# Optimization experiments

Hardware: AMD Instinct MI355X
Metric: run time of the kernel (lower is better)

Reference implementation:

```python
import jax, jax.numpy as jnp
import numpy as np

DIM = 1024
NUM_HEADS = 16
HEAD_DIM = DIM // NUM_HEADS
SCALE = DIM ** (-0.5)  # NOTE: original scales by full dim, not head_dim


def setup_inputs() -> dict:
    key = jax.random.key(0)
    ks = jax.random.split(key, 5)
    B, S = 2, 2048
    x = jax.random.normal(ks[0], (B, S, DIM), dtype=jnp.float32)
    w_qkv = jax.random.normal(ks[1], (DIM, 3 * DIM), dtype=jnp.float32) * (DIM ** -0.5)
    b_qkv = jax.random.normal(ks[2], (3 * DIM,), dtype=jnp.float32) * 0.02
    w_proj = jax.random.normal(ks[3], (DIM, DIM), dtype=jnp.float32) * (DIM ** -0.5)
    b_proj = jax.random.normal(ks[4], (DIM,), dtype=jnp.float32) * 0.02
    return {"x": x, "w_qkv": w_qkv, "b_qkv": b_qkv, "w_proj": w_proj, "b_proj": b_proj}


def reference(x, w_qkv, b_qkv, w_proj, b_proj):
    B, S, D = x.shape
    qkv = x @ w_qkv + b_qkv                                  # [B,S,3D]
    qkv = qkv.reshape(B, S, NUM_HEADS, 3 * HEAD_DIM).transpose(0, 2, 1, 3)  # [B,H,S,3hd]
    q, k, v = jnp.split(qkv, 3, axis=-1)                     # each [B,H,S,hd]
    attn = jnp.einsum("bhqd,bhkd->bhqk", q, k) * SCALE       # [B,H,S,S]
    attn = jax.nn.softmax(attn, axis=-1)
    out = jnp.einsum("bhqk,bhkd->bhqd", attn, v)             # [B,H,S,hd]
    out = out.transpose(0, 2, 1, 3).reshape(B, S, D)
    return out @ w_proj + b_proj
```

## Files before the change

### kernel.cpp

```cpp
#include <hip/hip_runtime.h>
#include <hip/hip_bf16.h>

#define DIM 1024
#define NH 16
#define HD 64
#define BB 2
#define SS 2048
#define MROWS (BB * SS)
#define SCALE 0.03125f
#define SC_LOG2E 0.04508422002778011f

typedef unsigned short u16;
typedef unsigned int u32;
typedef __attribute__((ext_vector_type(8))) short short8;
typedef __attribute__((ext_vector_type(4))) float f32x4;
typedef __attribute__((ext_vector_type(2))) unsigned int u32x2;

#if __has_builtin(__builtin_amdgcn_exp2f)
#define EXP2(x) __builtin_amdgcn_exp2f(x)
#else
#define EXP2(x) __builtin_exp2f(x)
#endif

__device__ __forceinline__ u16 f2bf(float f) {
  union { float f; u32 u; } v; v.f = f;
  return (u16)((v.u + 0x7fffu + ((v.u >> 16) & 1u)) >> 16);
}

__device__ __forceinline__ u32 pack2bf(float a, float b) {
  union { __hip_bfloat162 h; u32 u; } cv;
  cv.h = __float22bfloat162_rn(make_float2(a, b));
  return cv.u;
}

__device__ __forceinline__ void plswap32(u32& a, u32& b) {
#if __has_builtin(__builtin_amdgcn_permlane32_swap)
  u32x2 t = __builtin_amdgcn_permlane32_swap(a, b, false, false);
  a = t[0]; b = t[1];
#else
  asm("v_permlane32_swap_b32 %0, %1" : "+v"(a), "+v"(b));
#endif
}
__device__ __forceinline__ void plswap16(u32& a, u32& b) {
#if __has_builtin(__builtin_amdgcn_permlane16_swap)
  u32x2 t = __builtin_amdgcn_permlane16_swap(a, b, false, false);
  a = t[0]; b = t[1];
#else
  asm("v_permlane16_swap_b32 %0, %1" : "+v"(a), "+v"(b));
#endif
}

__device__ __forceinline__ void async16(const u16* g, u16* l) {
  __builtin_amdgcn_global_load_lds(
      (const __attribute__((address_space(1))) void*)(const void*)g,
      (__attribute__((address_space(3))) void*)(void*)l, 16, 0, 0);
}

__device__ __forceinline__ short8 ld8(const u16* p) { return *(const short8*)p; }

__global__ void cvt_kernel(const float* __restrict__ in, u16* __restrict__ out, int n4) {
  int i = blockIdx.x * blockDim.x + threadIdx.x;
  if (i < n4) {
    float4 v = ((const float4*)in)[i];
    u32 lo = (u32)f2bf(v.x) | ((u32)f2bf(v.y) << 16);
    u32 hi = (u32)f2bf(v.z) | ((u32)f2bf(v.w) << 16);
    ((uint2*)out)[i] = make_uint2(lo, hi);
  }
}

__global__ void tconv_kernel(const float* __restrict__ in, u16* __restrict__ out, int R, int C) {
  __shared__ u16 t[64 * 65];
  int c0 = blockIdx.x * 64, r0 = blockIdx.y * 64;
  #pragma unroll
  for (int i = 0; i < 16; i++) {
    int j = i * 256 + threadIdx.x;
    int rr = j >> 6, cc = j & 63;
    t[rr * 65 + cc] = f2bf(in[(size_t)(r0 + rr) * C + c0 + cc]);
  }
  __syncthreads();
  #pragma unroll
  for (int i = 0; i < 16; i++) {
    int j = i * 256 + threadIdx.x;
    int oc = j >> 6, orr = j & 63;
    out[(size_t)(c0 + oc) * R + r0 + orr] = t[orr * 65 + oc];
  }
}

template <int MODE, int BN, int NXB>
__global__ __launch_bounds__(256, (BN == 128 ? 2 : 3)) void gemm_bk64(
    const u16* __restrict__ A, const u16* __restrict__ Bt,
    const float* __restrict__ bias, void* __restrict__ C,
    u16* __restrict__ vT, int M, int N, int K) {
  constexpr int JN = BN / 32;
  constexpr int BTI = BN / 32;
  constexpr int BUF = 8192 + BN * 64;
  __shared__ __align__(16) u16 smem[2 * BUF];
  const int tid = threadIdx.x;
  const int w = tid >> 6, l = tid & 63;
  const int r = l & 15, q = l >> 4;
  const int nwg = gridDim.x;
  const int cpx = nwg >> 3;
  const int lin = blockIdx.x;
  const int swz = (lin & 7) * cpx + (lin >> 3);
  const int m0 = (swz / NXB) * 128, n0 = (swz % NXB) * BN;
  const int qm = (w & 1) * 64, qn = (w >> 1) * (BN / 2);

  const int gc = (l & 7) ^ (l >> 3);
  const size_t aoffb = (size_t)(m0 + w * 32 + (l >> 3)) * K + (size_t)gc * 8;
  const size_t boffb = (size_t)(n0 + w * (BN / 4) + (l >> 3)) * K + (size_t)gc * 8;
  const int xs = r & 7;

#define GSTAGE(K0, BASE) do {                                                    \
    u16* As_ = (BASE); u16* Bs_ = As_ + 8192;                                    \
    _Pragma("unroll")                                                            \
    for (int t = 0; t < 4; t++)                                                  \
      async16(A + aoffb + (size_t)t * 8 * K + (K0), As_ + w * 2048 + t * 512 + l * 8); \
    _Pragma("unroll")                                                            \
    for (int t = 0; t < BTI; t++)                                                \
      async16(Bt + boffb + (size_t)t * 8 * K + (K0), Bs_ + w * (BN * 16) + t * 512 + l * 8); \
  } while (0)

  f32x4 acc[4][JN] = {};
  GSTAGE(0, smem);
  __syncthreads();
  for (int k0 = 0; k0 < K; k0 += 64) {
    u16* As = smem + ((k0 >> 6) & 1) * BUF;
    u16* Bs = As + 8192;
    if (k0 + 64 < K) GSTAGE(k0 + 64, smem + ((((k0 >> 6) & 1) ^ 1) * BUF));
    short8 af[2][4], bfr[2][JN];
    #pragma unroll
    for (int kq = 0; kq < 2; kq++) {
      #pragma unroll
      for (int i = 0; i < 4; i++)
        af[kq][i] = ld8(&As[(qm + i * 16 + r) * 64 + (((kq * 4 + q) ^ xs) * 8)]);
      #pragma unroll
      for (int j = 0; j < JN; j++)
        bfr[kq][j] = ld8(&Bs[(qn + j * 16 + r) * 64 + (((kq * 4 + q) ^ xs) * 8)]);
    }
    #pragma unroll
    for (int kq = 0; kq < 2; kq++)
      #pragma unroll
      for (int i = 0; i < 4; i++)
        #pragma unroll
        for (int j = 0; j < JN; j++)
          acc[i][j] = __builtin_amdgcn_mfma_f32_16x16x32_bf16(af[kq][i], bfr[kq][j], acc[i][j], 0, 0, 0);
    __syncthreads();
  }
#undef GSTAGE
  #pragma unroll
  for (int i = 0; i < 4; i++) {
    int ro = m0 + qm + i * 16 + q * 4;
    #pragma unroll
    for (int j = 0; j < JN; j++) {
      int col = n0 + qn + j * 16 + r;
      float bv = bias[col];
      float v0 = acc[i][j][0] + bv, v1 = acc[i][j][1] + bv;
      float v2 = acc[i][j][2] + bv, v3 = acc[i][j][3] + bv;
      if (MODE == 1) {
        float* out = (float*)C;
        out[(size_t)(ro + 0) * N + col] = v0;
        out[(size_t)(ro + 1) * N + col] = v1;
        out[(size_t)(ro + 2) * N + col] = v2;
        out[(size_t)(ro + 3) * N + col] = v3;
      } else {
        int h = col / 192, wi = col - h * 192;
        if (wi >= 128) {
          int bb = ro >> 11, s = ro & 2047, d = wi - 128;
          uint2 pk = make_uint2(pack2bf(v0, v1), pack2bf(v2, v3));
          *(uint2*)&vT[((size_t)((bb * NH + h) * HD + d)) * SS + s] = pk;
        } else {
          u16* qk2 = (u16*)C;
          const float sc = (wi < 64) ? SC_LOG2E : 1.0f;
          qk2[(size_t)(ro + 0) * 2048 + h * 128 + wi] = f2bf(v0 * sc);
          qk2[(size_t)(ro + 1) * 2048 + h * 128 + wi] = f2bf(v1 * sc);
          qk2[(size_t)(ro + 2) * 2048 + h * 128 + wi] = f2bf(v2 * sc);
          qk2[(size_t)(ro + 3) * 2048 + h * 128 + wi] = f2bf(v3 * sc);
        }
      }
    }
  }
}

__global__ __launch_bounds__(512, 4) void attn6_kernel(
    const u16* __restrict__ qk2, const u16* __restrict__ vT,
    u16* __restrict__ attno) {
  __shared__ __align__(16) u16 smem[32768];
  const int tid = threadIdx.x;
  const int w = tid >> 6, l = tid & 63;
  const int r = l & 15, q = l >> 4;
  const int wq = w & 3, ws = w >> 2;
  const int lin = blockIdx.x + 16 * (blockIdx.y + 16 * blockIdx.z);
  const int k8 = lin & 7, jj = lin >> 3;
  const int bh = ((jj >> 4) << 3) + k8;
  const int h = bh & 15, b = bh >> 4;
  const int q0 = (jj & 15) * 128;

  const u16* qb = qk2 + (size_t)b * SS * 2048;
  const u16* kB = qb + h * 128 + 64;
  const u16* vB = vT + (size_t)((b * NH + h) * HD) * SS;

  short8 qf[2][2];
  #pragma unroll
  for (int i = 0; i < 2; i++)
    #pragma unroll
    for (int kq = 0; kq < 2; kq++)
      qf[i][kq] = ld8(qb + (size_t)(q0 + wq * 32 + i * 16 + r) * 2048 + h * 128 + kq * 32 + q * 8);

  const int klrow = l >> 3;
  const int kchunk = (l & 7) ^ klrow;
  const int vlrow = l >> 4;
  const int vslot = l & 15;

#define STAGE(KV0, DST) do {                                                     \
    u16* Kd_ = (DST); u16* Vd_ = Kd_ + 8192;                                     \
    _Pragma("unroll")                                                            \
    for (int tt = 0; tt < 2; tt++) {                                             \
      int g = w * 2 + tt;                                                        \
      async16(kB + (size_t)((KV0) + g * 8 + klrow) * 2048 + kchunk * 8,          \
              &Kd_[g * 512 + l * 8]);                                            \
    }                                                                            \
    _Pragma("unroll")                                                            \
    for (int tt = 0; tt < 2; tt++) {                                             \
      int g = w * 2 + tt;                                                        \
      int d_ = g * 4 + vlrow;                                                    \
      int c_ = vslot ^ (d_ & 15);                                                \
      async16(vB + (size_t)d_ * SS + (KV0) + c_ * 8, &Vd_[g * 512 + l * 8]);     \
    }                                                                            \
  } while (0)

#define CONV(ks) do {                                                            \
    _Pragma("unroll")                                                            \
    for (int i = 0; i < 2; i++) {                                                \
      f32x4 sa = sacc[(ks) * 2][i], sb = sacc[(ks) * 2 + 1][i];                  \
      u32 A0 = pack2bf(EXP2(sa[0]), EXP2(sa[1]));                                \
      u32 A1 = pack2bf(EXP2(sa[2]), EXP2(sa[3]));                                \
      u32 B0 = pack2bf(EXP2(sb[0]), EXP2(sb[1]));                                \
      u32 B1 = pack2bf(EXP2(sb[2]), EXP2(sb[3]));                                \
      plswap32(A0, B0);                                                          \
      plswap32(A1, B1);                                                          \
      plswap16(A0, B0);                                                          \
      plswap16(A1, B1);                                                          \
      union { short8 s8; u32 u[4]; } pk;                                         \
      pk.u[0] = A0; pk.u[1] = A1; pk.u[2] = B0; pk.u[3] = B1;                    \
      pa[ks][i] = pk.s8;                                                         \
    }                                                                            \
  } while (0)

#define QKT(j2) do {                                                             \
    const u16* krow = &Ks[(ws * 64 + (j2) * 16 + r) * 64];                       \
    short8 a0 = ld8(krow + ((q ^ (r & 7)) * 8));                                 \
    short8 a1 = ld8(krow + (((4 + q) ^ (r & 7)) * 8));                           \
    __builtin_amdgcn_s_setprio(1);                                               \
    _Pragma("unroll")                                                            \
    for (int i = 0; i < 2; i++) {                                                \
      sacc[j2][i] = __builtin_amdgcn_mfma_f32_16x16x32_bf16(a0, qf[i][0], sacc[j2][i], 0, 0, 0); \
      sacc[j2][i] = __builtin_amdgcn_mfma_f32_16x16x32_bf16(a1, qf[i][1], sacc[j2][i], 0, 0, 0); \
    }                                                                            \
    __builtin_amdgcn_s_setprio(0);                                               \
  } while (0)

#define PV(ks) do {                                                              \
    __builtin_amdgcn_s_setprio(1);                                               \
    den[0] = __builtin_amdgcn_mfma_f32_16x16x32_bf16(pa[ks][0], vone, den[0], 0, 0, 0); \
    den[1] = __builtin_amdgcn_mfma_f32_16x16x32_bf16(pa[ks][1], vone, den[1], 0, 0, 0); \
    _Pragma("unroll")                                                            \
    for (int dj = 0; dj < 4; dj++) {                                             \
      short8 vb = ld8(&Vs[(dj * 16 + r) * 128 + (((ws * 8 + (ks) * 4 + q) ^ r) * 8)]); \
      oacc[0][dj] = __builtin_amdgcn_mfma_f32_16x16x32_bf16(pa[ks][0], vb, oacc[0][dj], 0, 0, 0); \
      oacc[1][dj] = __builtin_amdgcn_mfma_f32_16x16x32_bf16(pa[ks][1], vb, oacc[1][dj], 0, 0, 0); \
    }                                                                            \
    __builtin_amdgcn_s_setprio(0);                                               \
  } while (0)

  const short8 vone = {0x3F80, 0x3F80, 0x3F80, 0x3F80, 0x3F80, 0x3F80, 0x3F80, 0x3F80};
  f32x4 oacc[2][4] = {};
  f32x4 den[2] = {};

  STAGE(0, smem);
  __syncthreads();

  for (int t = 0; t < 16; ++t) {
    const int cur = t & 1;
    u16* Ks = smem + cur * 16384;
    u16* Vs = Ks + 8192;
    if (t < 15) STAGE((t + 1) * 128, smem + (cur ^ 1) * 16384);

    f32x4 sacc[4][2] = {};
    short8 pa[2][2];
    QKT(0); QKT(1);
    CONV(0);
    QKT(2); QKT(3);
    PV(0);
    CONV(1);
    PV(1);
    __syncthreads();
  }
#undef STAGE
#undef CONV
#undef QKT
#undef PV

  float* part = (float*)smem;
  float* dnf  = part + 8 * 32 * 36;
  const int ho = 1 - ws;
  {
    const int wbase = (wq * 2 + ho) * 32;
    #pragma unroll
    for (int i = 0; i < 2; i++) {
      if (ws == 0) {
        *(f32x4*)&part[(wbase + r) * 36 + i * 16 + q * 4]      = oacc[i][2];
        *(f32x4*)&part[(wbase + 16 + r) * 36 + i * 16 + q * 4] = oacc[i][3];
      } else {
        *(f32x4*)&part[(wbase + r) * 36 + i * 16 + q * 4]      = oacc[i][0];
        *(f32x4*)&part[(wbase + 16 + r) * 36 + i * 16 + q * 4] = oacc[i][1];
      }
      if (r == 0)
        *(f32x4*)&dnf[(ws * 4 + wq) * 32 + i * 16 + q * 4] = den[i];
    }
  }
  __syncthreads();
  {
    const int rbase = (wq * 2 + ws) * 32;
    #pragma unroll
    for (int i = 0; i < 2; i++) {
      f32x4 dt = *(f32x4*)&dnf[(ho * 4 + wq) * 32 + i * 16 + q * 4] + den[i];
      f32x4 oa, ob;
      if (ws == 0) { oa = oacc[i][0]; ob = oacc[i][1]; }
      else         { oa = oacc[i][2]; ob = oacc[i][3]; }
      oa += *(f32x4*)&part[(rbase + r) * 36 + i * 16 + q * 4];
      ob += *(f32x4*)&part[(rbase + 16 + r) * 36 + i * 16 + q * 4];
      #pragma unroll
      for (int e = 0; e < 4; e++) {
        float di = 1.f / dt[e];
        int row = q0 + wq * 32 + i * 16 + q * 4 + e;
        u16* o = &attno[(size_t)(b * SS + row) * DIM + h * HD + ws * 32 + r];
        o[0]  = f2bf(oa[e] * di);
        o[16] = f2bf(ob[e] * di);
      }
    }
  }
}

extern "C" void kernel_launch(void* const* d_in, const int* in_sizes, int n_in,
                              void* d_out, int out_size, void* d_ws, size_t ws_size,
                              hipStream_t stream) {
  const float* x      = (const float*)d_in[0];
  const float* w_qkv  = (const float*)d_in[1];
  const float* b_qkv  = (const float*)d_in[2];
  const float* w_proj = (const float*)d_in[3];
  const float* b_proj = (const float*)d_in[4];
  float* out = (float*)d_out;
  char* ws = (char*)d_ws;
  u16* xb     = (u16*)(ws);
  u16* wqkvT  = (u16*)(ws + ((size_t)8  << 20));
  u16* wprojT = (u16*)(ws + ((size_t)14 << 20));
  u16* qk2    = (u16*)(ws + ((size_t)16 << 20));
  u16* attno  = (u16*)(ws + ((size_t)32 << 20));
  u16* vT     = (u16*)(ws + ((size_t)40 << 20));

  cvt_kernel<<<4096, 256, 0, stream>>>(x, xb, MROWS * DIM / 4);
  tconv_kernel<<<dim3(48, 16), 256, 0, stream>>>(w_qkv, wqkvT, DIM, 3 * DIM);
  tconv_kernel<<<dim3(16, 16), 256, 0, stream>>>(w_proj, wprojT, DIM, DIM);
  gemm_bk64<0, 128, 24><<<768, 256, 0, stream>>>(xb, wqkvT, b_qkv, qk2, vT, MROWS, 3 * DIM, DIM);
  attn6_kernel<<<dim3(16, NH, BB), 512, 0, stream>>>(qk2, vT, attno);
  gemm_bk64<1, 64, 16><<<512, 256, 0, stream>>>(attno, wprojT, b_proj, out, nullptr, MROWS, DIM, DIM);
}
```

Measured before the change: 177.0 us.

## Halve attention query and KV tiles to double block count and occupancy

The attention kernel now gives each block 64 query rows instead of 128 and streams 64-key tiles instead of 128, so the grid doubles to 1024 blocks. Shared memory per block drops to 32KB and launch bounds now request 8 blocks per CU, with simpler per-warp staging and a narrower partial-sum reduction. The aim is better occupancy and load balance, at the cost of less K/V reuse per block (twice the K/V reads overall), twice as many loop iterations and barriers, and less MFMA work between syncs. The softmax still has no running max, the same as before.

```diff
diff --git a/kernel.cpp b/kernel.cpp
--- a/kernel.cpp
+++ b/kernel.cpp
@@ -181,162 +181,118 @@
   }
 }
 
-__global__ __launch_bounds__(512, 4) void attn6_kernel(
+__global__ __launch_bounds__(512, 8) void attn7_kernel(
     const u16* __restrict__ qk2, const u16* __restrict__ vT,
     u16* __restrict__ attno) {
-  __shared__ __align__(16) u16 smem[32768];
+  __shared__ __align__(16) u16 smem[16384];
   const int tid = threadIdx.x;
   const int w = tid >> 6, l = tid & 63;
   const int r = l & 15, q = l >> 4;
   const int wq = w & 3, ws = w >> 2;
-  const int lin = blockIdx.x + 16 * (blockIdx.y + 16 * blockIdx.z);
+  const int lin = blockIdx.x + 32 * (blockIdx.y + 16 * blockIdx.z);
   const int k8 = lin & 7, jj = lin >> 3;
-  const int bh = ((jj >> 4) << 3) + k8;
+  const int bh = ((jj >> 5) << 3) + k8;
   const int h = bh & 15, b = bh >> 4;
-  const int q0 = (jj & 15) * 128;
+  const int q0 = (jj & 31) * 64;
 
   const u16* qb = qk2 + (size_t)b * SS * 2048;
   const u16* kB = qb + h * 128 + 64;
   const u16* vB = vT + (size_t)((b * NH + h) * HD) * SS;
 
-  short8 qf[2][2];
+  short8 qf[2];
   #pragma unroll
-  for (int i = 0; i < 2; i++)
-    #pragma unroll
-    for (int kq = 0; kq < 2; kq++)
-      qf[i][kq] = ld8(qb + (size_t)(q0 + wq * 32 + i * 16 + r) * 2048 + h * 128 + kq * 32 + q * 8);
-
-  const int klrow = l >> 3;
-  const int kchunk = (l & 7) ^ klrow;
-  const int vlrow = l >> 4;
-  const int vslot = l & 15;
+  for (int kq = 0; kq < 2; kq++)
+    qf[kq] = ld8(qb + (size_t)(q0 + wq * 16 + r) * 2048 + h * 128 + kq * 32 + q * 8);
+
+  const int gch = (l & 7) ^ (l >> 3);
 
 #define STAGE(KV0, DST) do {                                                     \
-    u16* Kd_ = (DST); u16* Vd_ = Kd_ + 8192;                                     \
-    _Pragma("unroll")                                                            \
-    for (int tt = 0; tt < 2; tt++) {                                             \
-      int g = w * 2 + tt;                                                        \
-      async16(kB + (size_t)((KV0) + g * 8 + klrow) * 2048 + kchunk * 8,          \
-              &Kd_[g * 512 + l * 8]);                                            \
-    }                                                                            \
-    _Pragma("unroll")                                                            \
-    for (int tt = 0; tt < 2; tt++) {                                             \
-      int g = w * 2 + tt;                                                        \
-      int d_ = g * 4 + vlrow;                                                    \
-      int c_ = vslot ^ (d_ & 15);                                                \
-      async16(vB + (size_t)d_ * SS + (KV0) + c_ * 8, &Vd_[g * 512 + l * 8]);     \
-    }                                                                            \
+    u16* Kd_ = (DST); u16* Vd_ = Kd_ + 4096;                                     \
+    async16(kB + (size_t)((KV0) + w * 8 + (l >> 3)) * 2048 + gch * 8,            \
+            &Kd_[w * 512 + l * 8]);                                              \
+    async16(vB + (size_t)(w * 8 + (l >> 3)) * SS + (KV0) + gch * 8,              \
+            &Vd_[w * 512 + l * 8]);                                              \
   } while (0)
 
-#define CONV(ks) do {                                                            \
-    _Pragma("unroll")                                                            \
-    for (int i = 0; i < 2; i++) {                                                \
-      f32x4 sa = sacc[(ks) * 2][i], sb = sacc[(ks) * 2 + 1][i];                  \
-      u32 A0 = pack2bf(EXP2(sa[0]), EXP2(sa[1]));                                \
-      u32 A1 = pack2bf(EXP2(sa[2]), EXP2(sa[3]));                                \
-      u32 B0 = pack2bf(EXP2(sb[0]), EXP2(sb[1]));                                \
-      u32 B1 = pack2bf(EXP2(sb[2]), EXP2(sb[3]));                                \
-      plswap32(A0, B0);                                                          \
-      plswap32(A1, B1);                                                          \
-      plswap16(A0, B0);                                                          \
-      plswap16(A1, B1);                                                          \
-      union { short8 s8; u32 u[4]; } pk;                                         \
-      pk.u[0] = A0; pk.u[1] = A1; pk.u[2] = B0; pk.u[3] = B1;                    \
-      pa[ks][i] = pk.s8;                                                         \
-    }                                                                            \
-  } while (0)
-
-#define QKT(j2) do {                                                             \
-    const u16* krow = &Ks[(ws * 64 + (j2) * 16 + r) * 64];                       \
-    short8 a0 = ld8(krow + ((q ^ (r & 7)) * 8));                                 \
-    short8 a1 = ld8(krow + (((4 + q) ^ (r & 7)) * 8));                           \
-    __builtin_amdgcn_s_setprio(1);                                               \
-    _Pragma("unroll")                                                            \
-    for (int i = 0; i < 2; i++) {                                                \
-      sacc[j2][i] = __builtin_amdgcn_mfma_f32_16x16x32_bf16(a0, qf[i][0], sacc[j2][i], 0, 0, 0); \
-      sacc[j2][i] = __builtin_amdgcn_mfma_f32_16x16x32_bf16(a1, qf[i][1], sacc[j2][i], 0, 0, 0); \
-    }                                                                            \
-    __builtin_amdgcn_s_setprio(0);                                               \
-  } while (0)
-
-#define PV(ks) do {                                                              \
-    __builtin_amdgcn_s_setprio(1);                                               \
-    den[0] = __builtin_amdgcn_mfma_f32_16x16x32_bf16(pa[ks][0], vone, den[0], 0, 0, 0); \
-    den[1] = __builtin_amdgcn_mfma_f32_16x16x32_bf16(pa[ks][1], vone, den[1], 0, 0, 0); \
-    _Pragma("unroll")                                                            \
-    for (int dj = 0; dj < 4; dj++) {                                             \
-      short8 vb = ld8(&Vs[(dj * 16 + r) * 128 + (((ws * 8 + (ks) * 4 + q) ^ r) * 8)]); \
-      oacc[0][dj] = __builtin_amdgcn_mfma_f32_16x16x32_bf16(pa[ks][0], vb, oacc[0][dj], 0, 0, 0); \
-      oacc[1][dj] = __builtin_amdgcn_mfma_f32_16x16x32_bf16(pa[ks][1], vb, oacc[1][dj], 0, 0, 0); \
-    }                                                                            \
-    __builtin_amdgcn_s_setprio(0);                                               \
-  } while (0)
-
   const short8 vone = {0x3F80, 0x3F80, 0x3F80, 0x3F80, 0x3F80, 0x3F80, 0x3F80, 0x3F80};
-  f32x4 oacc[2][4] = {};
-  f32x4 den[2] = {};
+  f32x4 oacc[4] = {};
+  f32x4 den = {};
 
   STAGE(0, smem);
   __syncthreads();
 
-  for (int t = 0; t < 16; ++t) {
-    const int cur = t & 1;
-    u16* Ks = smem + cur * 16384;
-    u16* Vs = Ks + 8192;
-    if (t < 15) STAGE((t + 1) * 128, smem + (cur ^ 1) * 16384);
-
-    f32x4 sacc[4][2] = {};
-    short8 pa[2][2];
-    QKT(0); QKT(1);
-    CONV(0);
-    QKT(2); QKT(3);
-    PV(0);
-    CONV(1);
-    PV(1);
+  for (int t = 0; t < 32; ++t) {
+    u16* Ks = smem + (t & 1) * 8192;
+    u16* Vs = Ks + 4096;
+    if (t < 31) STAGE((t + 1) * 64, smem + (((t & 1) ^ 1) * 8192));
+
+    f32x4 sacc[2] = {};
+    #pragma unroll
+    for (int j2 = 0; j2 < 2; j2++) {
+      const u16* krow = &Ks[(ws * 32 + j2 * 16 + r) * 64];
+      short8 a0 = ld8(krow + ((q ^ (r & 7)) * 8));
+      short8 a1 = ld8(krow + (((4 + q) ^ (r & 7)) * 8));
+      __builtin_amdgcn_s_setprio(1);
+      sacc[j2] = __builtin_amdgcn_mfma_f32_16x16x32_bf16(a0, qf[0], sacc[j2], 0, 0, 0);
+      sacc[j2] = __builtin_amdgcn_mfma_f32_16x16x32_bf16(a1, qf[1], sacc[j2], 0, 0, 0);
+      __builtin_amdgcn_s_setprio(0);
+    }
+    short8 pa;
+    {
+      u32 A0 = pack2bf(EXP2(sacc[0][0]), EXP2(sacc[0][1]));
+      u32 A1 = pack2bf(EXP2(sacc[0][2]), EXP2(sacc[0][3]));
+      u32 B0 = pack2bf(EXP2(sacc[1][0]), EXP2(sacc[1][1]));
+      u32 B1 = pack2bf(EXP2(sacc[1][2]), EXP2(sacc[1][3]));
+      plswap32(A0, B0);
+      plswap32(A1, B1);
+      plswap16(A0, B0);
+      plswap16(A1, B1);
+      union { short8 s8; u32 u[4]; } pk;
+      pk.u[0] = A0; pk.u[1] = A1; pk.u[2] = B0; pk.u[3] = B1;
+      pa = pk.s8;
+    }
+    __builtin_amdgcn_s_setprio(1);
+    den = __builtin_amdgcn_mfma_f32_16x16x32_bf16(pa, vone, den, 0, 0, 0);
+    #pragma unroll
+    for (int dj = 0; dj < 4; dj++) {
+      short8 vb = ld8(&Vs[(dj * 16 + r) * 64 + (((ws * 4 + q) ^ (r & 7)) * 8)]);
+      oacc[dj] = __builtin_amdgcn_mfma_f32_16x16x32_bf16(pa, vb, oacc[dj], 0, 0, 0);
+    }
+    __builtin_amdgcn_s_setprio(0);
     __syncthreads();
   }
 #undef STAGE
-#undef CONV
-#undef QKT
-#undef PV
 
   float* part = (float*)smem;
-  float* dnf  = part + 8 * 32 * 36;
+  float* dnf  = part + 8 * 32 * 20;
   const int ho = 1 - ws;
   {
     const int wbase = (wq * 2 + ho) * 32;
-    #pragma unroll
-    for (int i = 0; i < 2; i++) {
-      if (ws == 0) {
-        *(f32x4*)&part[(wbase + r) * 36 + i * 16 + q * 4]      = oacc[i][2];
-        *(f32x4*)&part[(wbase + 16 + r) * 36 + i * 16 + q * 4] = oacc[i][3];
-      } else {
-        *(f32x4*)&part[(wbase + r) * 36 + i * 16 + q * 4]      = oacc[i][0];
-        *(f32x4*)&part[(wbase + 16 + r) * 36 + i * 16 + q * 4] = oacc[i][1];
-      }
-      if (r == 0)
-        *(f32x4*)&dnf[(ws * 4 + wq) * 32 + i * 16 + q * 4] = den[i];
-    }
+    if (ws == 0) {
+      *(f32x4*)&part[(wbase + r) * 20 + q * 4]      = oacc[2];
+      *(f32x4*)&part[(wbase + 16 + r) * 20 + q * 4] = oacc[3];
+    } else {
+      *(f32x4*)&part[(wbase + r) * 20 + q * 4]      = oacc[0];
+      *(f32x4*)&part[(wbase + 16 + r) * 20 + q * 4] = oacc[1];
+    }
+    if (r == 0)
+      *(f32x4*)&dnf[(ws * 4 + wq) * 16 + q * 4] = den;
   }
   __syncthreads();
   {
     const int rbase = (wq * 2 + ws) * 32;
-    #pragma unroll
-    for (int i = 0; i < 2; i++) {
-      f32x4 dt = *(f32x4*)&dnf[(ho * 4 + wq) * 32 + i * 16 + q * 4] + den[i];
-      f32x4 oa, ob;
-      if (ws == 0) { oa = oacc[i][0]; ob = oacc[i][1]; }
-      else         { oa = oacc[i][2]; ob = oacc[i][3]; }
-      oa += *(f32x4*)&part[(rbase + r) * 36 + i * 16 + q * 4];
-      ob += *(f32x4*)&part[(rbase + 16 + r) * 36 + i * 16 + q * 4];
-      #pragma unroll
-      for (int e = 0; e < 4; e++) {
-        float di = 1.f / dt[e];
-        int row = q0 + wq * 32 + i * 16 + q * 4 + e;
-        u16* o = &attno[(size_t)(b * SS + row) * DIM + h * HD + ws * 32 + r];
-        o[0]  = f2bf(oa[e] * di);
-        o[16] = f2bf(ob[e] * di);
-      }
+    f32x4 dt = *(f32x4*)&dnf[(ho * 4 + wq) * 16 + q * 4] + den;
+    f32x4 oa = (ws == 0) ? oacc[0] : oacc[2];
+    f32x4 ob = (ws == 0) ? oacc[1] : oacc[3];
+    oa += *(f32x4*)&part[(rbase + r) * 20 + q * 4];
+    ob += *(f32x4*)&part[(rbase + 16 + r) * 20 + q * 4];
+    #pragma unroll
+    for (int e = 0; e < 4; e++) {
+      float di = 1.f / dt[e];
+      int row = q0 + wq * 16 + q * 4 + e;
+      u16* o = &attno[(size_t)(b * SS + row) * DIM + h * HD + ws * 32 + r];
+      o[0]  = f2bf(oa[e] * di);
+      o[16] = f2bf(ob[e] * di);
     }
   }
 }
@@ -362,6 +318,6 @@
   tconv_kernel<<<dim3(48, 16), 256, 0, stream>>>(w_qkv, wqkvT, DIM, 3 * DIM);
   tconv_kernel<<<dim3(16, 16), 256, 0, stream>>>(w_proj, wprojT, DIM, DIM);
   gemm_bk64<0, 128, 24><<<768, 256, 0, stream>>>(xb, wqkvT, b_qkv, qk2, vT, MROWS, 3 * DIM, DIM);
-  attn6_kernel<<<dim3(16, NH, BB), 512, 0, stream>>>(qk2, vT, attno);
+  attn7_kernel<<<dim3(32, NH, BB), 512, 0, stream>>>(qk2, vT, attno);
   gemm_bk64<1, 64, 16><<<512, 256, 0, stream>>>(attno, wprojT, b_proj, out, nullptr, MROWS, DIM, DIM);
 }
```

Measured after the change: 186.2 us. 1.05x slower.
